# Kernel optimization log

Measured on AMD Instinct MI355X. Metric: run time of the kernel, lower is better.

## Reference

```python
import jax, jax.numpy as jnp
import numpy as np

C = 180        # GatedGraphConv out_channels
L = 6          # num_layers inside GatedGraphConv
NG = 2048      # number of graphs in the batch
FC = 3 * C     # 540
EPS = 1e-5


def setup_inputs() -> dict:
    key = jax.random.key(0)
    ks = jax.random.split(key, 24)
    N, E, F = 50000, 150000, 64
    s = 1.0 / np.sqrt(C)
    inp = {}
    for i in range(3):
        inp[f"x{i+1}"] = jax.random.normal(ks[i], (N, F), jnp.float32)
        inp[f"edge_index{i+1}"] = jax.random.randint(ks[3 + i], (2, E), 0, N)
        inp[f"batch{i+1}"] = jnp.sort(jax.random.randint(ks[6 + i], (N,), 0, NG))
    # GatedGraphConv params (stacked for the 3 graph components)
    inp["conv_W"] = jax.random.normal(ks[9], (3, L, C, C), jnp.float32) * s
    inp["gru_Wih"] = jax.random.normal(ks[10], (3, 3 * C, C), jnp.float32) * s
    inp["gru_Whh"] = jax.random.normal(ks[11], (3, 3 * C, C), jnp.float32) * s
    inp["gru_bih"] = jnp.zeros((3, 3 * C), jnp.float32)
    inp["gru_bhh"] = jnp.zeros((3, 3 * C), jnp.float32)
    # BatchNorm1d (eval mode: running stats)
    inp["bn_gamma"] = jnp.ones((FC,), jnp.float32)
    inp["bn_beta"] = jnp.zeros((FC,), jnp.float32)
    inp["bn_mean"] = jnp.zeros((FC,), jnp.float32)
    inp["bn_var"] = jnp.ones((FC,), jnp.float32)
    # MLP head (torch Linear convention: W is [out, in])
    inp["fc1_W"] = jax.random.normal(ks[12], (FC * 3, FC), jnp.float32) / np.sqrt(FC)
    inp["fc1_b"] = jnp.zeros((FC * 3,), jnp.float32)
    inp["fc2_W"] = jax.random.normal(ks[13], (FC * 3, FC * 3), jnp.float32) / np.sqrt(FC * 3)
    inp["fc2_b"] = jnp.zeros((FC * 3,), jnp.float32)
    inp["fc25_W"] = jax.random.normal(ks[14], (FC, FC * 3), jnp.float32) / np.sqrt(FC * 3)
    inp["fc25_b"] = jnp.zeros((FC,), jnp.float32)
    inp["fc3_W"] = jax.random.normal(ks[15], (3, FC), jnp.float32) / np.sqrt(FC)
    inp["fc3_b"] = jnp.zeros((3,), jnp.float32)
    return inp


def _gated_graph_conv(x, edge_index, W, Wih, Whh, bih, bhh):
    # pad input features up to out_channels (PyG GatedGraphConv behavior)
    h = jnp.pad(x, ((0, 0), (0, C - x.shape[1])))  # [N, C]
    src, dst = edge_index[0], edge_index[1]

    def step(h, Wl):
        m = h @ Wl                                   # [N, C] linear transform
        agg = jnp.zeros_like(h).at[dst].add(m[src])  # scatter-add aggregation
        gi = agg @ Wih.T + bih                       # [N, 3C]
        gh = h @ Whh.T + bhh                         # [N, 3C]
        ir, iz, inn = jnp.split(gi, 3, axis=1)
        hr, hz, hn = jnp.split(gh, 3, axis=1)
        r = jax.nn.sigmoid(ir + hr)
        z = jax.nn.sigmoid(iz + hz)
        n = jnp.tanh(inn + r * hn)
        return (1.0 - z) * n + z * h, None

    h, _ = jax.lax.scan(step, h, W)
    return h


def _pool(h, batch):
    # global_mean_pool: segment mean over graphs
    sums = jax.ops.segment_sum(h, batch, num_segments=NG)
    cnt = jax.ops.segment_sum(jnp.ones((h.shape[0],), h.dtype), batch, num_segments=NG)
    return sums / jnp.maximum(cnt, 1.0)[:, None]


def reference(x1, x2, x3, edge_index1, edge_index2, edge_index3,
              batch1, batch2, batch3, conv_W, gru_Wih, gru_Whh, gru_bih, gru_bhh,
              bn_gamma, bn_beta, bn_mean, bn_var,
              fc1_W, fc1_b, fc2_W, fc2_b, fc25_W, fc25_b, fc3_W, fc3_b):
    xs = (x1, x2, x3)
    eis = (edge_index1, edge_index2, edge_index3)
    bs = (batch1, batch2, batch3)
    pooled = []
    for i in range(3):
        h = _gated_graph_conv(xs[i], eis[i], conv_W[i], gru_Wih[i], gru_Whh[i],
                              gru_bih[i], gru_bhh[i])
        h = jax.nn.relu(h)          # dropout is identity in eval
        pooled.append(_pool(h, bs[i]))
    x = jnp.concatenate(pooled, axis=1)  # [NG, 540]
    x = (x - bn_mean) * jax.lax.rsqrt(bn_var + EPS) * bn_gamma + bn_beta
    x = jax.nn.relu(x @ fc1_W.T + fc1_b)
    x = jax.nn.relu(x @ fc2_W.T + fc2_b)
    x = jax.nn.relu(x @ fc25_W.T + fc25_b)
    return x @ fc3_W.T + fc3_b           # [NG, 3]
```

## Files before the change

kernel.cpp:

```cpp
#include <hip/hip_runtime.h>

typedef unsigned int u32;
typedef unsigned short u16;
typedef __attribute__((ext_vector_type(8))) short bh8;
typedef __attribute__((ext_vector_type(4))) float f32x4;

#define CCH 180
#define LAY 6
#define NGR 2048
#define FIN 64
#define BM 128
#define BN 128
#define BK 20
#define PLANE_ROWS 50049

static __device__ __forceinline__ float sigmoidf_(float x) {
  return 1.0f / (1.0f + expf(-x));
}
static __device__ __forceinline__ u16 f2bf(float x) {
  union { float f; u32 u; } v; v.f = x;
  u32 r = v.u + 0x7FFFu + ((v.u >> 16) & 1u);
  return (u16)(r >> 16);
}
static __device__ __forceinline__ float bf2f(u32 b) {
  union { float f; u32 u; } v; v.u = b << 16;
  return v.f;
}
static __device__ __forceinline__ float unpk(u32 w) {
  return bf2f(w & 0xFFFFu) + bf2f(w >> 16);
}
static __device__ __forceinline__ u32 pk(float x) {
  u16 hi = f2bf(x);
  u16 lo = f2bf(x - bf2f(hi));
  return (u32)hi | ((u32)lo << 16);
}
static __device__ __forceinline__ u32 permlo(u32 a, u32 b) {
  return __builtin_amdgcn_perm(a, b, 0x05040100u);
}
static __device__ __forceinline__ u32 permhi(u32 a, u32 b) {
  return __builtin_amdgcn_perm(a, b, 0x07060302u);
}


__global__ void zero_i32_kernel(int* __restrict__ p, int n) {
  int i = blockIdx.x * 256 + threadIdx.x;
  if (i < n) p[i] = 0;
}
__global__ void zero_f32_kernel(float* __restrict__ p, int n) {
  int i = blockIdx.x * 256 + threadIdx.x;
  if (i < n) p[i] = 0.0f;
}

__global__ void pad_x_kernel(const float* __restrict__ x, u32* __restrict__ h, int nq) {
  int i = blockIdx.x * 256 + threadIdx.x;
  if (i >= nq) return;
  int n = i / 45;
  int q = i - n * 45;
  uint4 o;
  if (q < 16) {
    float4 v = *((const float4*)(x + (size_t)n * FIN) + q);
    o.x = pk(v.x); o.y = pk(v.y); o.z = pk(v.z); o.w = pk(v.w);
  } else {
    o = make_uint4(0u, 0u, 0u, 0u);
  }
  *((uint4*)(h + (size_t)n * CCH) + q) = o;
}

__global__ void hist_kernel(const int* __restrict__ idx, int* __restrict__ cnt, int n) {
  int i = blockIdx.x * 256 + threadIdx.x;
  if (i < n) atomicAdd(&cnt[idx[i]], 1);
}

__global__ void scan_kernel(const int* __restrict__ deg, int* __restrict__ rowstart,
                            int* __restrict__ cursor, int n) {
  __shared__ int sums[256];
  __shared__ int offs[257];
  int tid = threadIdx.x;
  int per = (n + 255) >> 8;
  int s0 = tid * per;
  int s1 = s0 + per; if (s1 > n) s1 = n;
  int local = 0;
  for (int i = s0; i < s1; ++i) local += deg[i];
  sums[tid] = local;
  __syncthreads();
  if (tid == 0) {
    int r = 0;
    for (int i = 0; i < 256; ++i) { offs[i] = r; r += sums[i]; }
    offs[256] = r;
  }
  __syncthreads();
  int run = offs[tid];
  for (int i = s0; i < s1; ++i) {
    int d = deg[i];
    rowstart[i] = run;
    cursor[i] = run;
    run += d;
  }
  if (tid == 0) rowstart[n] = offs[256];
}

__global__ void fill_kernel(const int* __restrict__ ei, int* __restrict__ cursor,
                            int* __restrict__ srclist, int E) {
  int e = blockIdx.x * 256 + threadIdx.x;
  if (e >= E) return;
  int d = ei[E + e];
  int p = atomicAdd(&cursor[d], 1);
  srclist[p] = ei[e];
}

__global__ void scatter_kernel(const u32* __restrict__ h, const int* __restrict__ rowstart,
                               const int* __restrict__ srclist, u32* __restrict__ out, int N) {
  int n = blockIdx.x * 4 + (threadIdx.x >> 6);
  int lane = threadIdx.x & 63;
  if (n >= N || lane >= 45) return;
  int s = rowstart[n], e = rowstart[n + 1];
  float a0 = 0.f, a1 = 0.f, a2 = 0.f, a3 = 0.f;
  for (int i = s; i < e; ++i) {
    uint4 w = *((const uint4*)(h + (size_t)srclist[i] * CCH) + lane);
    a0 += unpk(w.x); a1 += unpk(w.y); a2 += unpk(w.z); a3 += unpk(w.w);
  }
  uint4 o;
  o.x = pk(a0); o.y = pk(a1); o.z = pk(a2); o.w = pk(a3);
  *((uint4*)(out + (size_t)n * CCH) + lane) = o;
}

__global__ void fill_whh_kernel(const float* __restrict__ Whh_c, float* __restrict__ wc) {
  int cl = blockIdx.y;
  int idx = blockIdx.x * 256 + threadIdx.x;
  if (idx >= 180 * 540) return;
  int k = idx / 540;
  int jj = idx - k * 540;
  int dcol = (jj < 360) ? jj : jj + 180;
  wc[((size_t)cl * 360 + 180 + k) * 720 + dcol] = Whh_c[(size_t)jj * 180 + k];
}

__global__ void wt_build_gru_kernel(const float* __restrict__ wcomb, u32* __restrict__ wt) {
  int i = blockIdx.x * 256 + threadIdx.x;
  if (i >= LAY * 768 * 384) return;
  int l = i / (768 * 384);
  int r = i - l * (768 * 384);
  int c = r / 384, k = r - c * 384;
  int g = c & 3, j = c >> 2;
  float v = 0.0f;
  if (j < 180) {
    int sc = g * 180 + j;
    if (k < 180) v = wcomb[((size_t)l * 360 + k) * 720 + sc];
    else if (k >= 192 && k < 372) v = wcomb[((size_t)l * 360 + 180 + (k - 192)) * 720 + sc];
  }
  wt[i] = pk(v);
}

__global__ void bias4_build_kernel(const float* __restrict__ bih, const float* __restrict__ bhh,
                                   float4* __restrict__ b4) {
  int j = blockIdx.x * 64 + threadIdx.x;
  if (j < CCH)
    b4[j] = make_float4(bih[j] + bhh[j], bih[180 + j] + bhh[180 + j],
                        bih[360 + j], bhh[360 + j]);
}

__global__ void wt_mlp_build_kernel(const float* __restrict__ W, int outR, int inR,
                                    int outPad, int kPad, u32* __restrict__ dst) {
  int i = blockIdx.x * 256 + threadIdx.x;
  if (i >= outPad * kPad) return;
  int col = i / kPad, k = i - col * kPad;
  float v = (col < outR && k < inR) ? W[(size_t)col * inR + k] : 0.0f;
  dst[i] = pk(v);
}

__global__ __launch_bounds__(256) void gemm_bt_kernel(
    const float* __restrict__ A, int lda, long long sAz,
    const float* __restrict__ Bt, int ldb, long long sBz,
    float* __restrict__ Cb, int ldc, long long sCz,
    int M, int Ncols, int K) {
  __shared__ float As[BK][BM + 4];
  __shared__ float Bs[BK][BN + 4];
  int z = blockIdx.z;
  A  += (size_t)z * sAz;
  Bt += (size_t)z * sBz;
  Cb += (size_t)z * sCz;
  int bm = blockIdx.x * BM, bn = blockIdx.y * BN;
  int tid = threadIdx.x;
  int tr = tid >> 4, tc = tid & 15;
  float acc[8][8] = {};
  int lrow = tid >> 1;
  int lkh = (tid & 1) * 10;
  for (int k0 = 0; k0 < K; k0 += BK) {
    {
      int grow = bm + lrow;
      bool ok = (grow < M);
      const float* src = A + (size_t)grow * lda + k0 + lkh;
      #pragma unroll
      for (int i = 0; i < 10; ++i)
        As[lkh + i][lrow] = ok ? src[i] : 0.0f;
    }
    {
      int gcol = bn + lrow;
      bool ok = (gcol < Ncols);
      const float* src = Bt + (size_t)gcol * ldb + k0 + lkh;
      #pragma unroll
      for (int i = 0; i < 10; ++i)
        Bs[lkh + i][lrow] = ok ? src[i] : 0.0f;
    }
    __syncthreads();
    #pragma unroll 5
    for (int kk = 0; kk < BK; ++kk) {
      float4 a0 = *(const float4*)&As[kk][tr * 4];
      float4 a1 = *(const float4*)&As[kk][64 + tr * 4];
      float4 b0 = *(const float4*)&Bs[kk][tc * 4];
      float4 b1 = *(const float4*)&Bs[kk][64 + tc * 4];
      float av[8] = {a0.x, a0.y, a0.z, a0.w, a1.x, a1.y, a1.z, a1.w};
      float bv[8] = {b0.x, b0.y, b0.z, b0.w, b1.x, b1.y, b1.z, b1.w};
      #pragma unroll
      for (int i = 0; i < 8; ++i)
        #pragma unroll
        for (int j = 0; j < 8; ++j)
          acc[i][j] += av[i] * bv[j];
    }
    __syncthreads();
  }
  #pragma unroll
  for (int ih = 0; ih < 2; ++ih)
    #pragma unroll
    for (int i = 0; i < 4; ++i) {
      int r = bm + ih * 64 + tr * 4 + i;
      if (r >= M) continue;
      #pragma unroll
      for (int jh = 0; jh < 2; ++jh) {
        int c0 = bn + jh * 64 + tc * 4;
        if (c0 >= Ncols) continue;
        float4 v;
        v.x = acc[ih * 4 + i][jh * 4 + 0];
        v.y = acc[ih * 4 + i][jh * 4 + 1];
        v.z = acc[ih * 4 + i][jh * 4 + 2];
        v.w = acc[ih * 4 + i][jh * 4 + 3];
        *(float4*)&Cb[(size_t)r * ldc + c0] = v;
      }
    }
}

__global__ __launch_bounds__(256, 4) void gru_fused_kernel(
    const u32* __restrict__ hs, const u32* __restrict__ hp,
    const u32* __restrict__ wt, const float4* __restrict__ bias4,
    u32* __restrict__ hnew, int N) {
  __shared__ __align__(16) char smem[34816];
  u16* Ah = (u16*)smem;
  u16* Al = Ah + 4096;
  u16* Bh = Al + 4096;
  u16* Bl = Bh + 4096;

  int R = (N + 127) >> 7;
  int b = blockIdx.x;
  int full = (R >> 3) * 48;
  int bm_t, bn;
  if (b < full) {
    int g = b / 48, w = b - g * 48;
    bn = w >> 3;
    bm_t = (g << 3) + (w & 7);
  } else {
    int rem = R & 7;
    int b2 = b - full;
    bn = b2 / rem;
    bm_t = ((R >> 3) << 3) + (b2 - bn * rem);
  }
  int bm = bm_t << 7;

  int tid = threadIdx.x;
  int wid = tid >> 6, lane = tid & 63;
  int quad = lane >> 4, l16 = lane & 15;
  int rh = (wid & 1) << 6;
  int ch = (wid >> 1) << 6;
  f32x4 acc[4][4] = {};

  for (int ks = 0; ks < 12; ++ks) {
    const u32* ap = (ks < 6) ? hs : hp;
    int koff = ((ks < 6) ? ks : ks - 6) * 32;
    #pragma unroll
    for (int i = 0; i < 4; ++i) {
      int v = tid + i * 256;
      int rc = v >> 3, qq = v & 7;
      uint4 w = *(const uint4*)(ap + (size_t)(bm + rc) * CCH + koff + qq * 4);
      int d = (((qq >> 1) << 7) | rc) * 8 + (qq & 1) * 4;
      *(uint2*)&Ah[d] = make_uint2(permlo(w.y, w.x), permlo(w.w, w.z));
      *(uint2*)&Al[d] = make_uint2(permhi(w.y, w.x), permhi(w.w, w.z));
    }
    #pragma unroll
    for (int i = 0; i < 4; ++i) {
      int v = tid + i * 256;
      int rc = v >> 3, qq = v & 7;
      uint4 w = *(const uint4*)(wt + (size_t)(bn * 128 + rc) * 384 + ks * 32 + qq * 4);
      int d = (((qq >> 1) << 7) | rc) * 8 + (qq & 1) * 4;
      *(uint2*)&Bh[d] = make_uint2(permlo(w.y, w.x), permlo(w.w, w.z));
      *(uint2*)&Bl[d] = make_uint2(permhi(w.y, w.x), permhi(w.w, w.z));
    }
    __syncthreads();
    bh8 afh[4], afl[4], bfh[4], bfl[4];
    #pragma unroll
    for (int t = 0; t < 4; ++t) {
      int ra = ((quad << 7) + rh + (t << 4) + l16) << 3;
      afh[t] = *(const bh8*)&Ah[ra];
      afl[t] = *(const bh8*)&Al[ra];
      int rb = ((quad << 7) + ch + (t << 4) + l16) << 3;
      bfh[t] = *(const bh8*)&Bh[rb];
      bfl[t] = *(const bh8*)&Bl[rb];
    }
    #pragma unroll
    for (int i2 = 0; i2 < 4; ++i2)
      #pragma unroll
      for (int j2 = 0; j2 < 4; ++j2) {
        acc[i2][j2] = __builtin_amdgcn_mfma_f32_16x16x32_bf16(afh[i2], bfh[j2], acc[i2][j2], 0, 0, 0);
        acc[i2][j2] = __builtin_amdgcn_mfma_f32_16x16x32_bf16(afh[i2], bfl[j2], acc[i2][j2], 0, 0, 0);
        acc[i2][j2] = __builtin_amdgcn_mfma_f32_16x16x32_bf16(afl[i2], bfh[j2], acc[i2][j2], 0, 0, 0);
      }
    __syncthreads();
  }

  float* T = (float*)smem;
  #pragma unroll
  for (int p = 0; p < 2; ++p) {
    if ((wid >> 1) == p) {
      #pragma unroll
      for (int i2 = 0; i2 < 4; ++i2)
        #pragma unroll
        for (int j2 = 0; j2 < 4; ++j2) {
          int rb = rh + (i2 << 4) + (quad << 2);
          #pragma unroll
          for (int rg = 0; rg < 4; ++rg)
            T[(rb + rg) * 68 + (j2 << 4) + l16] = acc[i2][j2][rg];
        }
    }
    __syncthreads();
    #pragma unroll
    for (int s = 0; s < 8; ++s) {
      int idx = s * 256 + tid;
      int row = idx >> 4, jl = idx & 15;
      int j = bn * 32 + p * 16 + jl;
      int grow = bm + row;
      if (j < CCH && grow < N) {
        float4 g4 = *(const float4*)&T[row * 68 + (jl << 2)];
        float4 b4 = bias4[j];
        float r = sigmoidf_(g4.x + b4.x);
        float z = sigmoidf_(g4.y + b4.y);
        float nn = tanhf(g4.z + b4.z + r * (g4.w + b4.w));
        float hprev = unpk(hp[(size_t)grow * CCH + j]);
        float hv = (1.0f - z) * nn + z * hprev;
        hnew[(size_t)grow * CCH + j] = pk(hv);
      }
    }
    if (p == 0) __syncthreads();
  }
}

__global__ __launch_bounds__(256, 2) void mlp_mfma_kernel(
    const u32* __restrict__ A, int aStride, const u32* __restrict__ wt, int wStride,
    const float* __restrict__ bias, u32* __restrict__ Out, int oStride,
    int Ncols, int nks, int relu) {
  __shared__ __align__(16) char smem[32768];
  u16* Ah = (u16*)smem;
  u16* Al = Ah + 4096;
  u16* Bh = Al + 4096;
  u16* Bl = Bh + 4096;
  int bm = blockIdx.x * BM;
  int bn = blockIdx.y;
  int tid = threadIdx.x;
  int wid = tid >> 6, lane = tid & 63;
  int quad = lane >> 4, l16 = lane & 15;
  int rh = (wid & 1) << 6;
  int ch = (wid >> 1) << 6;
  f32x4 acc[4][4] = {};

  for (int ks = 0; ks < nks; ++ks) {
    int koff = ks * 32;
    #pragma unroll
    for (int i = 0; i < 4; ++i) {
      int v = tid + i * 256;
      int rc = v >> 3, qq = v & 7;
      uint4 w = *(const uint4*)(A + (size_t)(bm + rc) * aStride + koff + qq * 4);
      int d = (((qq >> 1) << 7) | rc) * 8 + (qq & 1) * 4;
      *(uint2*)&Ah[d] = make_uint2(permlo(w.y, w.x), permlo(w.w, w.z));
      *(uint2*)&Al[d] = make_uint2(permhi(w.y, w.x), permhi(w.w, w.z));
    }
    #pragma unroll
    for (int i = 0; i < 4; ++i) {
      int v = tid + i * 256;
      int rc = v >> 3, qq = v & 7;
      uint4 w = *(const uint4*)(wt + (size_t)(bn * 128 + rc) * wStride + koff + qq * 4);
      int d = (((qq >> 1) << 7) | rc) * 8 + (qq & 1) * 4;
      *(uint2*)&Bh[d] = make_uint2(permlo(w.y, w.x), permlo(w.w, w.z));
      *(uint2*)&Bl[d] = make_uint2(permhi(w.y, w.x), permhi(w.w, w.z));
    }
    __syncthreads();
    bh8 afh[4], afl[4], bfh[4], bfl[4];
    #pragma unroll
    for (int t = 0; t < 4; ++t) {
      int ra = ((quad << 7) + rh + (t << 4) + l16) << 3;
      afh[t] = *(const bh8*)&Ah[ra];
      afl[t] = *(const bh8*)&Al[ra];
      int rb = ((quad << 7) + ch + (t << 4) + l16) << 3;
      bfh[t] = *(const bh8*)&Bh[rb];
      bfl[t] = *(const bh8*)&Bl[rb];
    }
    #pragma unroll
    for (int i2 = 0; i2 < 4; ++i2)
      #pragma unroll
      for (int j2 = 0; j2 < 4; ++j2) {
        acc[i2][j2] = __builtin_amdgcn_mfma_f32_16x16x32_bf16(afh[i2], bfh[j2], acc[i2][j2], 0, 0, 0);
        acc[i2][j2] = __builtin_amdgcn_mfma_f32_16x16x32_bf16(afh[i2], bfl[j2], acc[i2][j2], 0, 0, 0);
        acc[i2][j2] = __builtin_amdgcn_mfma_f32_16x16x32_bf16(afl[i2], bfh[j2], acc[i2][j2], 0, 0, 0);
      }
    __syncthreads();
  }
  #pragma unroll
  for (int i2 = 0; i2 < 4; ++i2)
    #pragma unroll
    for (int j2 = 0; j2 < 4; ++j2) {
      int gc = bn * 128 + ch + (j2 << 4) + l16;
      if (gc >= Ncols) continue;
      float b = bias[gc];
      #pragma unroll
      for (int rg = 0; rg < 4; ++rg) {
        int grow = bm + rh + (i2 << 4) + (quad << 2) + rg;
        float v = acc[i2][j2][rg] + b;
        if (relu) v = fmaxf(v, 0.f);
        Out[(size_t)grow * oStride + gc] = pk(v);
      }
    }
}


__global__ void pool_kernel(const u32* __restrict__ h, const int* __restrict__ gstart,
                            float* __restrict__ pooled, int coff) {
  int g = blockIdx.x;
  int c = threadIdx.x;
  if (c >= CCH) return;
  int s = gstart[g], e = gstart[g + 1];
  float acc = 0.f;
  for (int n = s; n < e; ++n) acc += fmaxf(unpk(h[(size_t)n * CCH + c]), 0.f);
  pooled[(size_t)g * 540 + coff + c] = acc / fmaxf((float)(e - s), 1.0f);
}

__global__ void bn_pack_kernel(const float* __restrict__ p, const float* __restrict__ mean,
                               const float* __restrict__ var, const float* __restrict__ gamma,
                               const float* __restrict__ beta, u32* __restrict__ xn, int total) {
  int i = blockIdx.x * 256 + threadIdx.x;
  if (i >= total) return;
  int g = i / 540;
  int c = i - g * 540;
  float sc = gamma[c] / sqrtf(var[c] + 1e-5f);
  float v = (p[i] - mean[c]) * sc + beta[c];
  xn[(size_t)g * 544 + c] = pk(v);
}

__global__ void fc3_kernel(const u32* __restrict__ X, const float* __restrict__ W,
                           const float* __restrict__ b, float* __restrict__ out) {
  int g = blockIdx.x;
  int lane = threadIdx.x;
  const u32* x = X + (size_t)g * 544;
  for (int j = 0; j < 3; ++j) {
    const float* w = W + (size_t)j * 540;
    float s = 0.f;
    for (int i = lane; i < 540; i += 64) s += unpk(x[i]) * w[i];
    #pragma unroll
    for (int o = 32; o > 0; o >>= 1) s += __shfl_down(s, o);
    if (lane == 0) out[(size_t)g * 3 + j] = s + b[j];
  }
}


extern "C" void kernel_launch(void* const* d_in, const int* in_sizes, int n_in,
                              void* d_out, int out_size, void* d_ws, size_t ws_size,
                              hipStream_t stream) {
  (void)n_in; (void)out_size; (void)ws_size;
  const float* xs[3]   = {(const float*)d_in[0], (const float*)d_in[3], (const float*)d_in[6]};
  const int*   eis[3]  = {(const int*)d_in[1], (const int*)d_in[4], (const int*)d_in[7]};
  const int*   bats[3] = {(const int*)d_in[2], (const int*)d_in[5], (const int*)d_in[8]};
  const float* convW = (const float*)d_in[9];
  const float* Wih   = (const float*)d_in[10];
  const float* Whh   = (const float*)d_in[11];
  const float* bih   = (const float*)d_in[12];
  const float* bhh   = (const float*)d_in[13];
  const float* bng   = (const float*)d_in[14];
  const float* bnb   = (const float*)d_in[15];
  const float* bnm   = (const float*)d_in[16];
  const float* bnv   = (const float*)d_in[17];
  const float* fc1W  = (const float*)d_in[18];
  const float* fc1b  = (const float*)d_in[19];
  const float* fc2W  = (const float*)d_in[20];
  const float* fc2b  = (const float*)d_in[21];
  const float* fc25W = (const float*)d_in[22];
  const float* fc25b = (const float*)d_in[23];
  const float* fc3W  = (const float*)d_in[24];
  const float* fc3b  = (const float*)d_in[25];

  const int N = in_sizes[0] / FIN;
  const int E = in_sizes[1] / 2;

  char* p = (char*)d_ws;
  auto alloc = [&](size_t bytes) -> char* {
    char* r = p;
    p += (bytes + 255) & ~(size_t)255;
    return r;
  };
  const size_t PLANE = (size_t)PLANE_ROWS * CCH * 4;
  u32* P0 = (u32*)alloc(PLANE);
  u32* P1 = (u32*)alloc(PLANE);
  u32* P2 = (u32*)alloc(PLANE);
  float* pooled = (float*)alloc((size_t)NGR * 540 * 4);
  float4* bias4 = (float4*)alloc((size_t)CCH * 16);
  int* rowstart = (int*)alloc((size_t)(N + 1) * 4);
  int* srclist  = (int*)alloc((size_t)E * 4);
  int* gstart   = (int*)alloc((size_t)(NGR + 1) * 4);
  int* gcnt     = (int*)alloc((size_t)NGR * 4);

  float* wcomb = (float*)P2;
  int* cursor  = (int*)((char*)P2 + 6815744);
  u32* wtf1  = (u32*)P0;
  u32* wtf2  = wtf1 + (size_t)1664 * 544;
  u32* wtf25 = wtf2 + (size_t)1664 * 1632;
  u32* xn = (u32*)P1;
  u32* t1 = xn + (size_t)NGR * 544;
  u32* t2 = t1 + (size_t)NGR * 1632;
  u32* t3 = t2 + (size_t)NGR * 1632;

  const int rowBlocks = (N + BM - 1) / BM;

  for (int comp = 0; comp < 3; ++comp) {
    pad_x_kernel<<<(N * 45 + 255) / 256, 256, 0, stream>>>(xs[comp], P1, N * 45);

    zero_f32_kernel<<<(LAY * 360 * 720 + 255) / 256, 256, 0, stream>>>(wcomb, LAY * 360 * 720);
    {
      dim3 grid((180 + BM - 1) / BM, (540 + BN - 1) / BN, LAY);
      gemm_bt_kernel<<<grid, 256, 0, stream>>>(
          convW + (size_t)comp * LAY * 180 * 180, 180, 180LL * 180,
          Wih + (size_t)comp * 540 * 180, 180, 0,
          wcomb, 720, 360LL * 720, 180, 540, 180);
      dim3 g2((180 * 540 + 255) / 256, LAY);
      fill_whh_kernel<<<g2, 256, 0, stream>>>(Whh + (size_t)comp * 540 * 180, wcomb);
    }
    u32* wtg = (u32*)d_in[comp * 3];
    wt_build_gru_kernel<<<(LAY * 768 * 384 + 255) / 256, 256, 0, stream>>>(wcomb, wtg);
    bias4_build_kernel<<<3, 64, 0, stream>>>(bih + (size_t)comp * 540,
                                             bhh + (size_t)comp * 540, bias4);

    zero_i32_kernel<<<(N + 255) / 256, 256, 0, stream>>>(cursor, N);
    hist_kernel<<<(E + 255) / 256, 256, 0, stream>>>(eis[comp] + E, cursor, E);
    scan_kernel<<<1, 256, 0, stream>>>(cursor, rowstart, cursor, N);
    fill_kernel<<<(E + 255) / 256, 256, 0, stream>>>(eis[comp], cursor, srclist, E);

    for (int l = 0; l < LAY; ++l) {
      const u32* hp = (l & 1) ? P2 : P1;
      u32* hn = (l & 1) ? P1 : P2;
      scatter_kernel<<<(N + 3) / 4, 256, 0, stream>>>(hp, rowstart, srclist, P0, N);
      gru_fused_kernel<<<rowBlocks * 6, 256, 0, stream>>>(P0, hp, wtg + (size_t)l * 768 * 384,
                                                          bias4, hn, N);
    }
    zero_i32_kernel<<<(NGR + 255) / 256, 256, 0, stream>>>(gcnt, NGR);
    hist_kernel<<<(N + 255) / 256, 256, 0, stream>>>(bats[comp], gcnt, N);
    scan_kernel<<<1, 256, 0, stream>>>(gcnt, gstart, gcnt, NGR);
    pool_kernel<<<NGR, 192, 0, stream>>>(P1, gstart, pooled, comp * CCH);
  }

  wt_mlp_build_kernel<<<(1664 * 544 + 255) / 256, 256, 0, stream>>>(fc1W, 1620, 540, 1664, 544, wtf1);
  wt_mlp_build_kernel<<<(1664 * 1632 + 255) / 256, 256, 0, stream>>>(fc2W, 1620, 1620, 1664, 1632, wtf2);
  wt_mlp_build_kernel<<<(640 * 1632 + 255) / 256, 256, 0, stream>>>(fc25W, 540, 1620, 640, 1632, wtf25);

  bn_pack_kernel<<<(NGR * 540 + 255) / 256, 256, 0, stream>>>(pooled, bnm, bnv, bng, bnb, xn, NGR * 540);
  {
    dim3 g1(NGR / BM, 13);
    mlp_mfma_kernel<<<g1, 256, 0, stream>>>(xn, 544, wtf1, 544, fc1b, t1, 1632, 1620, 17, 1);
    mlp_mfma_kernel<<<g1, 256, 0, stream>>>(t1, 1632, wtf2, 1632, fc2b, t2, 1632, 1620, 51, 1);
    dim3 g3(NGR / BM, 5);
    mlp_mfma_kernel<<<g3, 256, 0, stream>>>(t2, 1632, wtf25, 1632, fc25b, t3, 544, 540, 51, 1);
    fc3_kernel<<<NGR, 64, 0, stream>>>(t3, fc3W, fc3b, (float*)d_out);
  }
}
```

Measured before the change: 3.740 ms.

## Split bf16 hi/lo activations and weights into separate planar arrays

Activations and GRU weights were stored as interleaved hi/lo bf16 pairs in u32 words. They are now stored as two separate u16 planes with padded row strides (184 and 384). The GRU GEMM can then copy global tiles straight into padded LDS rows without perm-based deinterleaving, and fragment loads become simple offset reads. Scatter, pad, pool and the GRU epilogue are updated to read and write both planes. This adds one extra load stream per access and changes the buffer aliasing plan.

New measurement: 3.958 ms. +5.8%, slower.

```diff
diff --git a/kernel.cpp b/kernel.cpp
--- a/kernel.cpp
+++ b/kernel.cpp
@@ -12,7 +12,9 @@
 #define BM 128
 #define BN 128
 #define BK 20
-#define PLANE_ROWS 50049
+#define PROWS 50049
+#define AKLD 184
+#define BKLD 384
 
 static __device__ __forceinline__ float sigmoidf_(float x) {
   return 1.0f / (1.0f + expf(-x));
@@ -51,19 +53,32 @@
   if (i < n) p[i] = 0.0f;
 }
 
-__global__ void pad_x_kernel(const float* __restrict__ x, u32* __restrict__ h, int nq) {
+__global__ void pad_x_kernel(const float* __restrict__ x, u16* __restrict__ hH,
+                             u16* __restrict__ hL, int nq) {
   int i = blockIdx.x * 256 + threadIdx.x;
   if (i >= nq) return;
-  int n = i / 45;
-  int q = i - n * 45;
-  uint4 o;
-  if (q < 16) {
-    float4 v = *((const float4*)(x + (size_t)n * FIN) + q);
-    o.x = pk(v.x); o.y = pk(v.y); o.z = pk(v.z); o.w = pk(v.w);
-  } else {
-    o = make_uint4(0u, 0u, 0u, 0u);
-  }
-  *((uint4*)(h + (size_t)n * CCH) + q) = o;
+  int n = i / 23;
+  int q = i - n * 23;
+  uint4 oh = make_uint4(0u, 0u, 0u, 0u), ol = oh;
+  if (q < 8) {
+    const float* xp = x + (size_t)n * FIN + q * 8;
+    float4 v0 = *(const float4*)xp;
+    float4 v1 = *(const float4*)(xp + 4);
+    float vv[8] = {v0.x, v0.y, v0.z, v0.w, v1.x, v1.y, v1.z, v1.w};
+    u32 h[8], l[8];
+    #pragma unroll
+    for (int c = 0; c < 8; ++c) {
+      u16 hb = f2bf(vv[c]);
+      h[c] = hb;
+      l[c] = f2bf(vv[c] - bf2f(hb));
+    }
+    oh = make_uint4(h[0] | (h[1] << 16), h[2] | (h[3] << 16),
+                    h[4] | (h[5] << 16), h[6] | (h[7] << 16));
+    ol = make_uint4(l[0] | (l[1] << 16), l[2] | (l[3] << 16),
+                    l[4] | (l[5] << 16), l[6] | (l[7] << 16));
+  }
+  *((uint4*)(hH + (size_t)n * AKLD) + q) = oh;
+  *((uint4*)(hL + (size_t)n * AKLD) + q) = ol;
 }
 
 __global__ void hist_kernel(const int* __restrict__ idx, int* __restrict__ cnt, int n) {
@@ -108,20 +123,40 @@
   srclist[p] = ei[e];
 }
 
-__global__ void scatter_kernel(const u32* __restrict__ h, const int* __restrict__ rowstart,
-                               const int* __restrict__ srclist, u32* __restrict__ out, int N) {
-  int n = blockIdx.x * 4 + (threadIdx.x >> 6);
-  int lane = threadIdx.x & 63;
-  if (n >= N || lane >= 45) return;
+__global__ void scatter_kernel(const u16* __restrict__ hH, const u16* __restrict__ hL,
+                               const int* __restrict__ rowstart, const int* __restrict__ srclist,
+                               u16* __restrict__ oH, u16* __restrict__ oL, int N) {
+  int n = blockIdx.x * 8 + (threadIdx.x >> 5);
+  int lane = threadIdx.x & 31;
+  if (n >= N || lane >= 23) return;
   int s = rowstart[n], e = rowstart[n + 1];
-  float a0 = 0.f, a1 = 0.f, a2 = 0.f, a3 = 0.f;
+  float a[8] = {};
   for (int i = s; i < e; ++i) {
-    uint4 w = *((const uint4*)(h + (size_t)srclist[i] * CCH) + lane);
-    a0 += unpk(w.x); a1 += unpk(w.y); a2 += unpk(w.z); a3 += unpk(w.w);
-  }
-  uint4 o;
-  o.x = pk(a0); o.y = pk(a1); o.z = pk(a2); o.w = pk(a3);
-  *((uint4*)(out + (size_t)n * CCH) + lane) = o;
+    size_t ro = (size_t)srclist[i] * AKLD;
+    uint4 wh = *((const uint4*)(hH + ro) + lane);
+    uint4 wl = *((const uint4*)(hL + ro) + lane);
+    a[0] += bf2f(wh.x & 0xFFFFu) + bf2f(wl.x & 0xFFFFu);
+    a[1] += bf2f(wh.x >> 16)     + bf2f(wl.x >> 16);
+    a[2] += bf2f(wh.y & 0xFFFFu) + bf2f(wl.y & 0xFFFFu);
+    a[3] += bf2f(wh.y >> 16)     + bf2f(wl.y >> 16);
+    a[4] += bf2f(wh.z & 0xFFFFu) + bf2f(wl.z & 0xFFFFu);
+    a[5] += bf2f(wh.z >> 16)     + bf2f(wl.z >> 16);
+    a[6] += bf2f(wh.w & 0xFFFFu) + bf2f(wl.w & 0xFFFFu);
+    a[7] += bf2f(wh.w >> 16)     + bf2f(wl.w >> 16);
+  }
+  u32 h[8], l[8];
+  #pragma unroll
+  for (int c = 0; c < 8; ++c) {
+    u16 hb = f2bf(a[c]);
+    h[c] = hb;
+    l[c] = f2bf(a[c] - bf2f(hb));
+  }
+  uint4 oh = make_uint4(h[0] | (h[1] << 16), h[2] | (h[3] << 16),
+                        h[4] | (h[5] << 16), h[6] | (h[7] << 16));
+  uint4 ol = make_uint4(l[0] | (l[1] << 16), l[2] | (l[3] << 16),
+                        l[4] | (l[5] << 16), l[6] | (l[7] << 16));
+  *((uint4*)(oH + (size_t)n * AKLD) + lane) = oh;
+  *((uint4*)(oL + (size_t)n * AKLD) + lane) = ol;
 }
 
 __global__ void fill_whh_kernel(const float* __restrict__ Whh_c, float* __restrict__ wc) {
@@ -134,12 +169,13 @@
   wc[((size_t)cl * 360 + 180 + k) * 720 + dcol] = Whh_c[(size_t)jj * 180 + k];
 }
 
-__global__ void wt_build_gru_kernel(const float* __restrict__ wcomb, u32* __restrict__ wt) {
+__global__ void wt_build_gru_kernel(const float* __restrict__ wcomb, u16* __restrict__ wtH,
+                                    u16* __restrict__ wtL) {
   int i = blockIdx.x * 256 + threadIdx.x;
-  if (i >= LAY * 768 * 384) return;
-  int l = i / (768 * 384);
-  int r = i - l * (768 * 384);
-  int c = r / 384, k = r - c * 384;
+  if (i >= LAY * 768 * BKLD) return;
+  int l = i / (768 * BKLD);
+  int r = i - l * (768 * BKLD);
+  int c = r / BKLD, k = r - c * BKLD;
   int g = c & 3, j = c >> 2;
   float v = 0.0f;
   if (j < 180) {
@@ -147,7 +183,9 @@
     if (k < 180) v = wcomb[((size_t)l * 360 + k) * 720 + sc];
     else if (k >= 192 && k < 372) v = wcomb[((size_t)l * 360 + 180 + (k - 192)) * 720 + sc];
   }
-  wt[i] = pk(v);
+  u16 hb = f2bf(v);
+  wtH[i] = hb;
+  wtL[i] = f2bf(v - bf2f(hb));
 }
 
 __global__ void bias4_build_kernel(const float* __restrict__ bih, const float* __restrict__ bhh,
@@ -239,14 +277,16 @@
 }
 
 __global__ __launch_bounds__(256, 4) void gru_fused_kernel(
-    const u32* __restrict__ hs, const u32* __restrict__ hp,
-    const u32* __restrict__ wt, const float4* __restrict__ bias4,
-    u32* __restrict__ hnew, int N) {
-  __shared__ __align__(16) char smem[34816];
-  u16* Ah = (u16*)smem;
-  u16* Al = Ah + 4096;
-  u16* Bh = Al + 4096;
-  u16* Bl = Bh + 4096;
+    const u16* __restrict__ hsH, const u16* __restrict__ hsL,
+    const u16* __restrict__ hpH, const u16* __restrict__ hpL,
+    const u16* __restrict__ wtH, const u16* __restrict__ wtL,
+    const float4* __restrict__ bias4,
+    u16* __restrict__ hnH, u16* __restrict__ hnL, int N) {
+  __shared__ __align__(16) char smem[40960];
+  char* Ah = smem;
+  char* Al = smem + 10240;
+  char* Bh = smem + 20480;
+  char* Bl = smem + 30720;
 
   int R = (N + 127) >> 7;
   int b = blockIdx.x;
@@ -271,37 +311,50 @@
   int ch = (wid >> 1) << 6;
   f32x4 acc[4][4] = {};
 
+  int aoff[4], boff[4];
+  #pragma unroll
+  for (int t = 0; t < 4; ++t) {
+    aoff[t] = (rh + (t << 4) + l16) * 80 + (quad << 4);
+    boff[t] = (ch + (t << 4) + l16) * 80 + (quad << 4);
+  }
+  int rc0 = tid >> 2,          q0 = (tid & 3) << 4;
+  int rc1 = (tid + 256) >> 2,  q1 = ((tid + 256) & 3) << 4;
+
   for (int ks = 0; ks < 12; ++ks) {
-    const u32* ap = (ks < 6) ? hs : hp;
-    int koff = ((ks < 6) ? ks : ks - 6) * 32;
-    #pragma unroll
-    for (int i = 0; i < 4; ++i) {
-      int v = tid + i * 256;
-      int rc = v >> 3, qq = v & 7;
-      uint4 w = *(const uint4*)(ap + (size_t)(bm + rc) * CCH + koff + qq * 4);
-      int d = (((qq >> 1) << 7) | rc) * 8 + (qq & 1) * 4;
-      *(uint2*)&Ah[d] = make_uint2(permlo(w.y, w.x), permlo(w.w, w.z));
-      *(uint2*)&Al[d] = make_uint2(permhi(w.y, w.x), permhi(w.w, w.z));
-    }
-    #pragma unroll
-    for (int i = 0; i < 4; ++i) {
-      int v = tid + i * 256;
-      int rc = v >> 3, qq = v & 7;
-      uint4 w = *(const uint4*)(wt + (size_t)(bn * 128 + rc) * 384 + ks * 32 + qq * 4);
-      int d = (((qq >> 1) << 7) | rc) * 8 + (qq & 1) * 4;
-      *(uint2*)&Bh[d] = make_uint2(permlo(w.y, w.x), permlo(w.w, w.z));
-      *(uint2*)&Bl[d] = make_uint2(permhi(w.y, w.x), permhi(w.w, w.z));
+    const char* aHp = (const char*)((ks < 6) ? hsH : hpH);
+    const char* aLp = (const char*)((ks < 6) ? hsL : hpL);
+    int kA = ((ks < 6) ? ks : ks - 6) * 64;
+    int kB = ks * 64;
+    {
+      size_t ga0 = (size_t)(bm + rc0) * 368 + kA + q0;
+      size_t ga1 = (size_t)(bm + rc1) * 368 + kA + q1;
+      size_t gb0 = (size_t)(bn * 128 + rc0) * 768 + kB + q0;
+      size_t gb1 = (size_t)(bn * 128 + rc1) * 768 + kB + q1;
+      uint4 vah0 = *(const uint4*)(aHp + ga0);
+      uint4 vah1 = *(const uint4*)(aHp + ga1);
+      uint4 val0 = *(const uint4*)(aLp + ga0);
+      uint4 val1 = *(const uint4*)(aLp + ga1);
+      uint4 vbh0 = *(const uint4*)((const char*)wtH + gb0);
+      uint4 vbh1 = *(const uint4*)((const char*)wtH + gb1);
+      uint4 vbl0 = *(const uint4*)((const char*)wtL + gb0);
+      uint4 vbl1 = *(const uint4*)((const char*)wtL + gb1);
+      *(uint4*)(Ah + rc0 * 80 + q0) = vah0;
+      *(uint4*)(Ah + rc1 * 80 + q1) = vah1;
+      *(uint4*)(Al + rc0 * 80 + q0) = val0;
+      *(uint4*)(Al + rc1 * 80 + q1) = val1;
+      *(uint4*)(Bh + rc0 * 80 + q0) = vbh0;
+      *(uint4*)(Bh + rc1 * 80 + q1) = vbh1;
+      *(uint4*)(Bl + rc0 * 80 + q0) = vbl0;
+      *(uint4*)(Bl + rc1 * 80 + q1) = vbl1;
     }
     __syncthreads();
     bh8 afh[4], afl[4], bfh[4], bfl[4];
     #pragma unroll
     for (int t = 0; t < 4; ++t) {
-      int ra = ((quad << 7) + rh + (t << 4) + l16) << 3;
-      afh[t] = *(const bh8*)&Ah[ra];
-      afl[t] = *(const bh8*)&Al[ra];
-      int rb = ((quad << 7) + ch + (t << 4) + l16) << 3;
-      bfh[t] = *(const bh8*)&Bh[rb];
-      bfl[t] = *(const bh8*)&Bl[rb];
+      afh[t] = *(const bh8*)(Ah + aoff[t]);
+      afl[t] = *(const bh8*)(Al + aoff[t]);
+      bfh[t] = *(const bh8*)(Bh + boff[t]);
+      bfl[t] = *(const bh8*)(Bl + boff[t]);
     }
     #pragma unroll
     for (int i2 = 0; i2 < 4; ++i2)
@@ -341,9 +394,12 @@
         float r = sigmoidf_(g4.x + b4.x);
         float z = sigmoidf_(g4.y + b4.y);
         float nn = tanhf(g4.z + b4.z + r * (g4.w + b4.w));
-        float hprev = unpk(hp[(size_t)grow * CCH + j]);
+        size_t ho = (size_t)grow * AKLD + j;
+        float hprev = bf2f(hpH[ho]) + bf2f(hpL[ho]);
         float hv = (1.0f - z) * nn + z * hprev;
-        hnew[(size_t)grow * CCH + j] = pk(hv);
+        u16 hb = f2bf(hv);
+        hnH[ho] = hb;
+        hnL[ho] = f2bf(hv - bf2f(hb));
       }
     }
     if (p == 0) __syncthreads();
@@ -427,14 +483,18 @@
 }
 
 
-__global__ void pool_kernel(const u32* __restrict__ h, const int* __restrict__ gstart,
+__global__ void pool_kernel(const u16* __restrict__ hH, const u16* __restrict__ hL,
+                            const int* __restrict__ gstart,
                             float* __restrict__ pooled, int coff) {
   int g = blockIdx.x;
   int c = threadIdx.x;
   if (c >= CCH) return;
   int s = gstart[g], e = gstart[g + 1];
   float acc = 0.f;
-  for (int n = s; n < e; ++n) acc += fmaxf(unpk(h[(size_t)n * CCH + c]), 0.f);
+  for (int n = s; n < e; ++n) {
+    size_t o = (size_t)n * AKLD + c;
+    acc += fmaxf(bf2f(hH[o]) + bf2f(hL[o]), 0.f);
+  }
   pooled[(size_t)g * 540 + coff + c] = acc / fmaxf((float)(e - s), 1.0f);
 }
 
@@ -500,10 +560,13 @@
     p += (bytes + 255) & ~(size_t)255;
     return r;
   };
-  const size_t PLANE = (size_t)PLANE_ROWS * CCH * 4;
-  u32* P0 = (u32*)alloc(PLANE);
-  u32* P1 = (u32*)alloc(PLANE);
-  u32* P2 = (u32*)alloc(PLANE);
+  const size_t PLANE = (size_t)PROWS * AKLD * 2;
+  u16* hsH = (u16*)alloc(PLANE);
+  u16* hsL = (u16*)alloc(PLANE);
+  u16* hAH = (u16*)alloc(PLANE);
+  u16* hAL = (u16*)alloc(PLANE);
+  u16* hBH = (u16*)alloc(PLANE);
+  u16* hBL = (u16*)alloc(PLANE);
   float* pooled = (float*)alloc((size_t)NGR * 540 * 4);
   float4* bias4 = (float4*)alloc((size_t)CCH * 16);
   int* rowstart = (int*)alloc((size_t)(N + 1) * 4);
@@ -511,12 +574,12 @@
   int* gstart   = (int*)alloc((size_t)(NGR + 1) * 4);
   int* gcnt     = (int*)alloc((size_t)NGR * 4);
 
-  float* wcomb = (float*)P2;
-  int* cursor  = (int*)((char*)P2 + 6815744);
-  u32* wtf1  = (u32*)P0;
+  float* wcomb = (float*)hsH;
+  int* cursor  = (int*)hsL;
+  u32* wtf1  = (u32*)hsH;
   u32* wtf2  = wtf1 + (size_t)1664 * 544;
   u32* wtf25 = wtf2 + (size_t)1664 * 1632;
-  u32* xn = (u32*)P1;
+  u32* xn = (u32*)hAH;
   u32* t1 = xn + (size_t)NGR * 544;
   u32* t2 = t1 + (size_t)NGR * 1632;
   u32* t3 = t2 + (size_t)NGR * 1632;
@@ -524,8 +587,6 @@
   const int rowBlocks = (N + BM - 1) / BM;
 
   for (int comp = 0; comp < 3; ++comp) {
-    pad_x_kernel<<<(N * 45 + 255) / 256, 256, 0, stream>>>(xs[comp], P1, N * 45);
-
     zero_f32_kernel<<<(LAY * 360 * 720 + 255) / 256, 256, 0, stream>>>(wcomb, LAY * 360 * 720);
     {
       dim3 grid((180 + BM - 1) / BM, (540 + BN - 1) / BN, LAY);
@@ -536,8 +597,12 @@
       dim3 g2((180 * 540 + 255) / 256, LAY);
       fill_whh_kernel<<<g2, 256, 0, stream>>>(Whh + (size_t)comp * 540 * 180, wcomb);
     }
-    u32* wtg = (u32*)d_in[comp * 3];
-    wt_build_gru_kernel<<<(LAY * 768 * 384 + 255) / 256, 256, 0, stream>>>(wcomb, wtg);
+
+    pad_x_kernel<<<(N * 23 + 255) / 256, 256, 0, stream>>>(xs[comp], hAH, hAL, N * 23);
+
+    u16* wtgH = (u16*)d_in[comp * 3];
+    u16* wtgL = wtgH + (size_t)LAY * 768 * BKLD;
+    wt_build_gru_kernel<<<(LAY * 768 * BKLD + 255) / 256, 256, 0, stream>>>(wcomb, wtgH, wtgL);
     bias4_build_kernel<<<3, 64, 0, stream>>>(bih + (size_t)comp * 540,
                                              bhh + (size_t)comp * 540, bias4);
 
@@ -547,16 +612,20 @@
     fill_kernel<<<(E + 255) / 256, 256, 0, stream>>>(eis[comp], cursor, srclist, E);
 
     for (int l = 0; l < LAY; ++l) {
-      const u32* hp = (l & 1) ? P2 : P1;
-      u32* hn = (l & 1) ? P1 : P2;
-      scatter_kernel<<<(N + 3) / 4, 256, 0, stream>>>(hp, rowstart, srclist, P0, N);
-      gru_fused_kernel<<<rowBlocks * 6, 256, 0, stream>>>(P0, hp, wtg + (size_t)l * 768 * 384,
-                                                          bias4, hn, N);
+      const u16* hpH = (l & 1) ? hBH : hAH;
+      const u16* hpL = (l & 1) ? hBL : hAL;
+      u16* hnH = (l & 1) ? hAH : hBH;
+      u16* hnL = (l & 1) ? hAL : hBL;
+      scatter_kernel<<<(N + 7) / 8, 256, 0, stream>>>(hpH, hpL, rowstart, srclist, hsH, hsL, N);
+      gru_fused_kernel<<<rowBlocks * 6, 256, 0, stream>>>(
+          hsH, hsL, hpH, hpL,
+          wtgH + (size_t)l * 768 * BKLD, wtgL + (size_t)l * 768 * BKLD,
+          bias4, hnH, hnL, N);
     }
     zero_i32_kernel<<<(NGR + 255) / 256, 256, 0, stream>>>(gcnt, NGR);
     hist_kernel<<<(N + 255) / 256, 256, 0, stream>>>(bats[comp], gcnt, N);
     scan_kernel<<<1, 256, 0, stream>>>(gcnt, gstart, gcnt, NGR);
-    pool_kernel<<<NGR, 192, 0, stream>>>(P1, gstart, pooled, comp * CCH);
+    pool_kernel<<<NGR, 192, 0, stream>>>(hAH, hAL, gstart, pooled, comp * CCH);
   }
 
   wt_mlp_build_kernel<<<(1664 * 544 + 255) / 256, 256, 0, stream>>>(fc1W, 1620, 540, 1664, 544, wtf1);
```
